# Optimization experiments

Hardware: AMD Instinct MI355X
Metric: run time of the kernel (lower is better)

Reference implementation:

```python
import jax, jax.numpy as jnp
import numpy as np

# PEPS grid configuration (matches init_kwargs)
X, Y = 4, 4            # xnodes, ynodes
D = 6                  # bond_dim
P = 2                  # features_in (physical dim)
F = 10                 # features_out (forced by result.view([10]))
CX, CY = X // 2, Y // 2  # center node carries the output leg
BATCH = 2048


def node_labels(i, j):
    # bond labels after the physical index is contracted away; axis order: up, left, down, right, out
    labs = []
    if i > 0: labs.append(f'v{i-1}_{j}')   # up bond (shared with row i-1)
    if j > 0: labs.append(f'h{i}_{j-1}')   # left bond (shared with col j-1)
    if i < X - 1: labs.append(f'v{i}_{j}') # down bond
    if j < Y - 1: labs.append(f'h{i}_{j}') # right bond
    if (i, j) == (CX, CY): labs.append('o')  # output leg on center node
    return labs


def node_shape(i, j):
    shp = [P]  # physical axis first (input_nodes[i][j][0] ^ peps_nodes[i][j][0])
    shp += [D] * (int(i > 0) + int(j > 0) + int(i < X - 1) + int(j < Y - 1))
    if (i, j) == (CX, CY): shp.append(F)
    return tuple(shp)


def setup_inputs() -> dict:
    key = jax.random.key(0)
    keys = jax.random.split(key, X * Y + 1)
    inp = {"x": jax.random.normal(keys[0], (BATCH, X, Y, P), dtype=jnp.float32)}
    k = 1
    for i in range(X):
        for j in range(Y):
            # simple_peps uniform init with std=0.01
            inp[f"w{i}{j}"] = jax.random.uniform(keys[k], node_shape(i, j), dtype=jnp.float32, minval=-0.01, maxval=0.01)
            k += 1
    return inp


def _td(a, alabs, b, blabs):
    """Label-tracked tensordot over all shared bond labels."""
    shared = [l for l in alabs if l in blabs]
    ai = [alabs.index(l) for l in shared]
    bi = [blabs.index(l) for l in shared]
    out = jnp.tensordot(a, b, axes=(ai, bi))
    labs = [l for l in alabs if l not in shared] + [l for l in blabs if l not in shared]
    return out, labs


def _contract_sample(xs, ws):
    # xs: [X, Y, P] one sample; ws: list-of-lists of node tensors
    # 1) contract each input vector into its PEPS node over the physical axis,
    #    then L2-normalize each contracted node (as in func())
    nodes = []
    for i in range(X):
        row = []
        for j in range(Y):
            t = jnp.tensordot(xs[i, j], ws[i][j], axes=(0, 0))
            t = t / jnp.linalg.norm(t)
            row.append(t)
        nodes.append(row)
    # 2) exact contraction of the 2D network, row-by-row boundary sweep
    cur, labs = nodes[0][0], node_labels(0, 0)
    for j in range(1, Y):
        cur, labs = _td(cur, labs, nodes[0][j], node_labels(0, j))
    for i in range(1, X):
        for j in range(Y):
            cur, labs = _td(cur, labs, nodes[i][j], node_labels(i, j))
    out = cur.reshape(F)  # result.view([10])
    return out / jnp.linalg.norm(out)


def reference(x, w00, w01, w02, w03, w10, w11, w12, w13,
              w20, w21, w22, w23, w30, w31, w32, w33):
    ws = [[w00, w01, w02, w03],
          [w10, w11, w12, w13],
          [w20, w21, w22, w23],
          [w30, w31, w32, w33]]
    return jax.vmap(lambda s: _contract_sample(s, ws))(x)  # [B, F]
```

## Files before the change

### kernel.cpp

```cpp
#include <hip/hip_runtime.h>
#include <math.h>

#define NT 128
#define NTG 256

struct PW { const float* w[16]; int perp[16]; };

__global__ __launch_bounds__(NTG) void gram16(PW pw, float* __restrict__ g) {
    const int n = blockIdx.x;
    const float* __restrict__ W = pw.w[n];
    const int m = pw.perp[n];
    float s00 = 0.f, s01 = 0.f, s11 = 0.f;
    for (int e = threadIdx.x; e < m; e += NTG) {
        float a = W[e], b = W[m + e];
        s00 += a * a; s01 += a * b; s11 += b * b;
    }
    for (int off = 32; off > 0; off >>= 1) {
        s00 += __shfl_down(s00, off, 64);
        s01 += __shfl_down(s01, off, 64);
        s11 += __shfl_down(s11, off, 64);
    }
    __shared__ float red[4][3];
    const int lane = threadIdx.x & 63, wv = threadIdx.x >> 6;
    if (lane == 0) { red[wv][0] = s00; red[wv][1] = s01; red[wv][2] = s11; }
    __syncthreads();
    if (threadIdx.x == 0) {
        float t0 = 0.f, t1 = 0.f, t2 = 0.f;
        for (int i = 0; i < 4; i++) { t0 += red[i][0]; t1 += red[i][1]; t2 += red[i][2]; }
        g[n * 3 + 0] = t0; g[n * 3 + 1] = t1; g[n * 3 + 2] = t2;
    }
}

constexpr int BA = 0, BB = 1296, BC = 2592, BD = 3888;
constexpr int PBo = 5184, SA = 5400, SB = 5616, SC = 5832;
constexpr int ASZ = 5868;

template<int M, int DST>
__device__ __forceinline__ void tmat(float* __restrict__ lds, const float* __restrict__ W,
                                     float al, float be, int tid) {
    for (int e = tid; e < M; e += NT) lds[DST + e] = al * W[e] + be * W[M + e];
}

template<int X1, int X2, int Y1, int Y2, int U, int L, int TX,
         int AX1, int AX2, int AU, int AL,
         int BU, int BLS, int BY1, int BY2,
         int OX1, int OX2, int OY1, int OY2,
         int AOFF, int BOFF, int OOFF>
__device__ __forceinline__ void step(float* __restrict__ lds, int tid) {
    constexpr int XB = X2 / TX;
    constexpr int TILES = X1 * XB * Y1;
    for (int r = tid; r < TILES; r += NT) {
        const int x1 = r / (XB * Y1);
        const int rm = r - x1 * (XB * Y1);
        const int xb = rm / Y1;
        const int y1 = rm - xb * Y1;
        const float* __restrict__ Ab = lds + AOFF + x1 * AX1 + xb * TX * AX2;
        const float* __restrict__ Bb = lds + BOFF + y1 * BY1;
        float acc[TX][Y2];
#pragma unroll
        for (int i = 0; i < TX; i++)
#pragma unroll
            for (int t2 = 0; t2 < Y2; t2++) acc[i][t2] = 0.f;
#pragma unroll
        for (int u = 0; u < U; u++) {
#pragma unroll
            for (int l = 0; l < L; l++) {
                float a[TX];
#pragma unroll
                for (int i = 0; i < TX; i++) a[i] = Ab[i * AX2 + u * AU + l * AL];
                const float* __restrict__ Bp = Bb + u * BU + l * BLS;
#pragma unroll
                for (int t2 = 0; t2 < Y2; t2++) {
                    const float bv = Bp[t2 * BY2];
#pragma unroll
                    for (int i = 0; i < TX; i++) acc[i][t2] += a[i] * bv;
                }
            }
        }
        float* __restrict__ Ob = lds + OOFF + x1 * OX1 + xb * TX * OX2 + y1 * OY1;
#pragma unroll
        for (int i = 0; i < TX; i++)
#pragma unroll
            for (int t2 = 0; t2 < Y2; t2++) Ob[i * OX2 + t2 * OY2] = acc[i][t2];
    }
}

__global__ __launch_bounds__(NT) void peps_main(const float* __restrict__ x, PW pw,
                                                const float* __restrict__ gram,
                                                float* __restrict__ out) {
    __shared__ float lds[ASZ];
    __shared__ float cfa[16], cfb[16];
    __shared__ float red[2][10];

    const int tid = threadIdx.x;
    const int s = blockIdx.x;

    if (tid < 16) {
        const float a = x[s * 32 + tid * 2 + 0];
        const float b = x[s * 32 + tid * 2 + 1];
        const float g0 = gram[tid * 3 + 0], g1 = gram[tid * 3 + 1], g2 = gram[tid * 3 + 2];
        const float inv = 1.f / sqrtf(a * a * g0 + 2.f * a * b * g1 + b * b * g2);
        cfa[tid] = a * inv; cfb[tid] = b * inv;
    }
    __syncthreads();

#define TM(M, DST, WI) tmat<M, DST>(lds, pw.w[WI], cfa[WI], cfb[WI], tid)
#define SYNC __syncthreads()

    TM(36, SC, 0); TM(216, SA, 1); SYNC;
    step<1, 6, 6, 6, 6, 1, 1,  0, 6, 1, 0,   36, 0, 6, 1,   0, 36, 6, 1,  SC, SA, PBo>(lds, tid);
    TM(216, SB, 4); SYNC;
    step<1, 36, 6, 6, 6, 1, 2,  0, 1, 36, 0,  36, 0, 6, 1,   0, 36, 6, 1,  PBo, SB, BA>(lds, tid);
    TM(1296, BB, 5); SYNC;
    step<6, 6, 6, 6, 6, 6, 2,  36, 6, 216, 1, 216, 36, 6, 1, 216, 36, 6, 1, BA, BB, BC>(lds, tid);
    TM(216, SA, 2); TM(36, SC, 3); SYNC;
    step<1, 36, 1, 6, 6, 1, 1,  0, 6, 1, 0,   6, 0, 0, 1,    0, 6, 0, 1,   SA, SC, PBo>(lds, tid);
    TM(216, SB, 7); SYNC;
    step<1, 36, 6, 6, 6, 1, 2,  0, 6, 1, 0,   36, 0, 6, 1,   0, 36, 6, 1,  PBo, SB, BA>(lds, tid);
    TM(1296, BB, 6); SYNC;
    step<6, 6, 6, 6, 6, 6, 2,  36, 6, 216, 1, 36, 6, 216, 1, 216, 36, 6, 1, BB, BA, BD>(lds, tid);
    TM(36, SC, 12); TM(216, SA, 8); SYNC;
    step<6, 6, 6, 6, 6, 6, 2,  36, 6, 216, 1, 6, 216, 36, 1, 216, 36, 6, 1, BC, BD, BA>(lds, tid);
    step<1, 6, 6, 6, 6, 1, 1,  0, 1, 6, 0,    6, 0, 36, 1,   0, 36, 6, 1,  SC, SA, PBo>(lds, tid);
    TM(216, SB, 13); SYNC;
    step<1, 36, 6, 6, 6, 1, 2,  0, 1, 36, 0,  6, 0, 36, 1,   0, 36, 6, 1,  PBo, SB, BC>(lds, tid);
    TM(1296, BD, 9); SYNC;
    step<6, 6, 6, 6, 6, 6, 2,  216, 1, 36, 6, 36, 6, 216, 1, 216, 36, 6, 1, BC, BD, BB>(lds, tid);
    TM(216, SA, 11); TM(36, SC, 15); SYNC;
    step<6, 6, 6, 6, 6, 6, 2,  6, 1, 216, 36, 216, 6, 36, 1, 216, 36, 6, 1, BA, BB, BC>(lds, tid);
    step<6, 6, 1, 6, 6, 1, 1,  36, 6, 1, 0,   6, 0, 0, 1,    36, 6, 0, 1,  SA, SC, PBo>(lds, tid);
    TM(216, SB, 14); SYNC;
    step<6, 6, 6, 6, 6, 1, 2,  36, 6, 1, 0,   1, 0, 36, 6,   216, 1, 6, 36, PBo, SB, BA>(lds, tid);
    SYNC;
    step<6, 6, 6, 6, 6, 6, 2,  216, 1, 36, 6, 216, 36, 6, 1, 216, 36, 6, 1, BC, BA, BB>(lds, tid);
    SYNC;
#undef TM
#undef SYNC

    {
        const float al = cfa[10], be = cfb[10];
        const float* __restrict__ w0 = pw.w[10];
        const float* __restrict__ w1 = w0 + 12960;
        float p[10];
#pragma unroll
        for (int o = 0; o < 10; o++) p[o] = 0.f;
        for (int e = tid; e < 1296; e += NT) {
            const float Ev = lds[BB + e];
            const float* __restrict__ q0 = w0 + e * 10;
            const float* __restrict__ q1 = w1 + e * 10;
#pragma unroll
            for (int o = 0; o < 10; o++) p[o] += Ev * (al * q0[o] + be * q1[o]);
        }
#pragma unroll
        for (int o = 0; o < 10; o++)
            for (int off = 32; off > 0; off >>= 1)
                p[o] += __shfl_down(p[o], off, 64);
        const int lane = tid & 63, wv = tid >> 6;
        if (lane == 0) {
#pragma unroll
            for (int o = 0; o < 10; o++) red[wv][o] = p[o];
        }
        __syncthreads();
        if (tid == 0) {
            float r[10];
            float ss = 0.f;
#pragma unroll
            for (int o = 0; o < 10; o++) {
                r[o] = red[0][o] + red[1][o];
                ss += r[o] * r[o];
            }
            const float inv = 1.f / sqrtf(ss);
#pragma unroll
            for (int o = 0; o < 10; o++) out[s * 10 + o] = r[o] * inv;
        }
    }
}

extern "C" void kernel_launch(void* const* d_in, const int* in_sizes, int n_in,
                              void* d_out, int out_size, void* d_ws, size_t ws_size,
                              hipStream_t stream) {
    PW pw;
    for (int k = 0; k < 16; k++) {
        pw.w[k] = (const float*)d_in[1 + k];
        pw.perp[k] = in_sizes[1 + k] / 2;
    }
    float* gram = (float*)d_ws;
    gram16<<<16, NTG, 0, stream>>>(pw, gram);

    const float* x = (const float*)d_in[0];
    const int B = out_size / 10;
    peps_main<<<B, NT, 0, stream>>>(x, pw, gram, (float*)d_out);
}
```

Measured before the change: 159.4 us.

## Precompute per-quadrant corner tables over physical-index combinations, then combine per sample

Adds a tables kernel that contracts each 4-node corner quadrant for all 16 (or 8) combinations of physical-index choices, using only the weights. Each sample then rebuilds its corner boundary tensors as a linear combination of these tables, weighted by products of its normalized input coefficients, and finishes with three 36x36x36 matmuls, handling two samples per block. This replaces most of the per-sample chained contractions with table reads and dense matmuls. The cost is a larger workspace read from global memory per sample and an extra launch.

```diff
diff --git a/kernel.cpp b/kernel.cpp
--- a/kernel.cpp
+++ b/kernel.cpp
@@ -5,6 +5,11 @@
 #define NTG 256
 
 struct PW { const float* w[16]; int perp[16]; };
+
+#define TLT 64
+#define TRT 20800
+#define BLT 41536
+#define RTT 62272
 
 __global__ __launch_bounds__(NTG) void gram16(PW pw, float* __restrict__ g) {
     const int n = blockIdx.x;
@@ -31,121 +36,219 @@
     }
 }
 
-constexpr int BA = 0, BB = 1296, BC = 2592, BD = 3888;
-constexpr int PBo = 5184, SA = 5400, SB = 5616, SC = 5832;
-constexpr int ASZ = 5868;
+template<int X1, int X2, int Y1, int Y2, int U, int L,
+         int AX1, int AX2, int AU, int AL,
+         int BU, int BLs, int BY1, int BY2,
+         int OX1, int OX2, int OY1, int OY2>
+__device__ __forceinline__ void contract(const float* __restrict__ A,
+                                         const float* __restrict__ Bm,
+                                         float* __restrict__ O, int tid) {
+    constexpr int ROWS = X1 * X2 * Y1;
+    for (int r = tid; r < ROWS; r += NT) {
+        const int x1 = r / (X2 * Y1);
+        const int rm = r - x1 * (X2 * Y1);
+        const int x2 = rm / Y1;
+        const int y1 = rm - x2 * Y1;
+        const float* __restrict__ Ab = A + x1 * AX1 + x2 * AX2;
+        const float* __restrict__ Bb = Bm + y1 * BY1;
+        float acc[Y2];
+#pragma unroll
+        for (int t = 0; t < Y2; t++) acc[t] = 0.f;
+#pragma unroll
+        for (int u = 0; u < U; u++) {
+#pragma unroll
+            for (int l = 0; l < L; l++) {
+                const float a = Ab[u * AU + l * AL];
+                const float* __restrict__ Bp = Bb + u * BU + l * BLs;
+#pragma unroll
+                for (int t = 0; t < Y2; t++) acc[t] += a * Bp[t * BY2];
+            }
+        }
+        float* __restrict__ Ob = O + x1 * OX1 + x2 * OX2 + y1 * OY1;
+#pragma unroll
+        for (int t = 0; t < Y2; t++) Ob[t * OY2] = acc[t];
+    }
+}
 
 template<int M, int DST>
-__device__ __forceinline__ void tmat(float* __restrict__ lds, const float* __restrict__ W,
-                                     float al, float be, int tid) {
-    for (int e = tid; e < M; e += NT) lds[DST + e] = al * W[e] + be * W[M + e];
-}
-
-template<int X1, int X2, int Y1, int Y2, int U, int L, int TX,
-         int AX1, int AX2, int AU, int AL,
-         int BU, int BLS, int BY1, int BY2,
-         int OX1, int OX2, int OY1, int OY2,
-         int AOFF, int BOFF, int OOFF>
-__device__ __forceinline__ void step(float* __restrict__ lds, int tid) {
-    constexpr int XB = X2 / TX;
-    constexpr int TILES = X1 * XB * Y1;
-    for (int r = tid; r < TILES; r += NT) {
-        const int x1 = r / (XB * Y1);
-        const int rm = r - x1 * (XB * Y1);
-        const int xb = rm / Y1;
-        const int y1 = rm - xb * Y1;
-        const float* __restrict__ Ab = lds + AOFF + x1 * AX1 + xb * TX * AX2;
-        const float* __restrict__ Bb = lds + BOFF + y1 * BY1;
-        float acc[TX][Y2];
-#pragma unroll
-        for (int i = 0; i < TX; i++)
-#pragma unroll
-            for (int t2 = 0; t2 < Y2; t2++) acc[i][t2] = 0.f;
-#pragma unroll
-        for (int u = 0; u < U; u++) {
-#pragma unroll
-            for (int l = 0; l < L; l++) {
-                float a[TX];
-#pragma unroll
-                for (int i = 0; i < TX; i++) a[i] = Ab[i * AX2 + u * AU + l * AL];
-                const float* __restrict__ Bp = Bb + u * BU + l * BLS;
-#pragma unroll
-                for (int t2 = 0; t2 < Y2; t2++) {
-                    const float bv = Bp[t2 * BY2];
-#pragma unroll
-                    for (int i = 0; i < TX; i++) acc[i][t2] += a[i] * bv;
-                }
+__device__ __forceinline__ void csel(float* __restrict__ L, const float* __restrict__ W, int tid) {
+    for (int e = tid; e < M; e += NT) L[DST + e] = W[e];
+}
+
+__global__ __launch_bounds__(NT) void tables_k(PW pw, float* __restrict__ ws) {
+    __shared__ float L[4356];
+    constexpr int bA = 0, bB = 1296, bC = 2592, sA = 3888, sB = 4104, sC = 4320;
+    const int tid = threadIdx.x, bid = blockIdx.x;
+    if (bid < 16) {
+        const int p = bid;
+        csel<36, sC>(L, pw.w[0] + ((p >> 0) & 1) * 36, tid);
+        csel<216, sA>(L, pw.w[1] + ((p >> 1) & 1) * 216, tid);
+        __syncthreads();
+        contract<1,6,6,6,6,1,  0,6,1,0,  36,0,6,1,  0,36,6,1>(L+sC, L+sA, L+sB, tid);
+        csel<216, bA>(L, pw.w[4] + ((p >> 2) & 1) * 216, tid);
+        __syncthreads();
+        contract<1,36,6,6,6,1,  0,1,36,0,  36,0,6,1,  0,36,6,1>(L+sB, L+bA, L+bB, tid);
+        csel<1296, bC>(L, pw.w[5] + ((p >> 3) & 1) * 1296, tid);
+        __syncthreads();
+        contract<6,6,6,6,6,6,  36,6,216,1,  216,36,6,1,  216*16,6*16,1*16,36*16>(L+bB, L+bC, ws + TLT + p, tid);
+    } else if (bid < 32) {
+        const int p = bid - 16;
+        csel<216, sA>(L, pw.w[2] + ((p >> 0) & 1) * 216, tid);
+        csel<36, sC>(L, pw.w[3] + ((p >> 1) & 1) * 36, tid);
+        __syncthreads();
+        contract<1,36,1,6,6,1,  0,6,1,0,  6,0,0,1,  0,6,0,1>(L+sA, L+sC, L+sB, tid);
+        csel<216, bA>(L, pw.w[7] + ((p >> 2) & 1) * 216, tid);
+        __syncthreads();
+        contract<1,36,6,6,6,1,  0,6,1,0,  36,0,6,1,  0,36,6,1>(L+sB, L+bA, L+bB, tid);
+        csel<1296, bC>(L, pw.w[6] + ((p >> 3) & 1) * 1296, tid);
+        __syncthreads();
+        contract<6,6,6,6,6,6,  36,6,216,1,  36,6,216,1,  36*16,6*16,216*16,1*16>(L+bC, L+bB, ws + TRT + p, tid);
+    } else if (bid < 48) {
+        const int p = bid - 32;
+        csel<36, sC>(L, pw.w[12] + ((p >> 0) & 1) * 36, tid);
+        csel<216, sA>(L, pw.w[8] + ((p >> 1) & 1) * 216, tid);
+        __syncthreads();
+        contract<1,6,6,6,6,1,  0,1,6,0,  6,0,36,1,  0,36,6,1>(L+sC, L+sA, L+sB, tid);
+        csel<216, bA>(L, pw.w[13] + ((p >> 2) & 1) * 216, tid);
+        __syncthreads();
+        contract<1,36,6,6,6,1,  0,1,36,0,  6,0,36,1,  0,36,6,1>(L+sB, L+bA, L+bB, tid);
+        csel<1296, bC>(L, pw.w[9] + ((p >> 3) & 1) * 1296, tid);
+        __syncthreads();
+        contract<6,6,6,6,6,6,  216,1,36,6,  36,6,216,1,  216*16,1*16,36*16,6*16>(L+bB, L+bC, ws + BLT + p, tid);
+    } else {
+        const int p = bid - 48;
+        csel<216, sA>(L, pw.w[11] + ((p >> 0) & 1) * 216, tid);
+        csel<36, sC>(L, pw.w[15] + ((p >> 1) & 1) * 36, tid);
+        __syncthreads();
+        contract<6,6,1,6,6,1,  36,6,1,0,  6,0,0,1,  36,6,0,1>(L+sA, L+sC, L+sB, tid);
+        csel<216, bA>(L, pw.w[14] + ((p >> 2) & 1) * 216, tid);
+        __syncthreads();
+        contract<6,6,6,6,6,1,  36,6,1,0,  1,0,36,6,  216*8,1*8,6*8,36*8>(L+sB, L+bA, ws + RTT + p, tid);
+    }
+}
+
+constexpr int AR = 5184;
+
+template<int PC, int DST, int GOFF>
+__device__ __forceinline__ void sweep(float* __restrict__ lds, const float* __restrict__ tab,
+                                      const float* __restrict__ gam, int tid) {
+    float g0[PC], g1[PC];
+#pragma unroll
+    for (int c = 0; c < PC; c++) { g0[c] = gam[GOFF + c]; g1[c] = gam[56 + GOFF + c]; }
+    for (int e = tid; e < 1296; e += NT) {
+        const float4* __restrict__ tp = (const float4*)(tab + e * PC);
+        float a0 = 0.f, a1 = 0.f;
+#pragma unroll
+        for (int c = 0; c < PC / 4; c++) {
+            const float4 v = tp[c];
+            a0 += v.x * g0[4*c] + v.y * g0[4*c+1] + v.z * g0[4*c+2] + v.w * g0[4*c+3];
+            a1 += v.x * g1[4*c] + v.y * g1[4*c+1] + v.z * g1[4*c+2] + v.w * g1[4*c+3];
+        }
+        lds[DST + e] = a0;
+        lds[AR + DST + e] = a1;
+    }
+}
+
+template<int SXH, int SXL, int SYH, int SYL, int AOFF, int BOFF, int OOFF>
+__device__ __forceinline__ void kmm(float* __restrict__ lds, int tid) {
+    for (int t = tid; t < 108; t += NT) {
+        const int sl = t / 54;
+        const int r = t - sl * 54;
+        const int xg = r / 3, yg = r - xg * 3;
+        const int x0 = xg * 2, y0 = yg * 12;
+        const float* __restrict__ A = lds + sl * AR + AOFF;
+        const float* __restrict__ B = lds + sl * AR + BOFF;
+        float acc0[12], acc1[12];
+#pragma unroll
+        for (int j = 0; j < 12; j++) { acc0[j] = 0.f; acc1[j] = 0.f; }
+#pragma unroll
+        for (int k = 0; k < 36; k++) {
+            const float2 a = *(const float2*)(A + k * 36 + x0);
+            const float* __restrict__ Bp = B + k * 36 + y0;
+            const float4 v0 = *(const float4*)(Bp);
+            const float4 v1 = *(const float4*)(Bp + 4);
+            const float4 v2 = *(const float4*)(Bp + 8);
+            const float bv[12] = {v0.x,v0.y,v0.z,v0.w, v1.x,v1.y,v1.z,v1.w, v2.x,v2.y,v2.z,v2.w};
+#pragma unroll
+            for (int j = 0; j < 12; j++) {
+                acc0[j] += a.x * bv[j];
+                acc1[j] += a.y * bv[j];
             }
         }
-        float* __restrict__ Ob = lds + OOFF + x1 * OX1 + xb * TX * OX2 + y1 * OY1;
-#pragma unroll
-        for (int i = 0; i < TX; i++)
-#pragma unroll
-            for (int t2 = 0; t2 < Y2; t2++) Ob[i * OX2 + t2 * OY2] = acc[i][t2];
+        float* __restrict__ O = lds + sl * AR + OOFF;
+#pragma unroll
+        for (int i = 0; i < 2; i++) {
+            const int xx = x0 + i;
+            const int xh = xx / 6, xl = xx - xh * 6;
+#pragma unroll
+            for (int j = 0; j < 12; j++) {
+                const int yy = y0 + j;
+                const int yh = yy / 6, yl = yy - yh * 6;
+                O[xh * SXH + xl * SXL + yh * SYH + yl * SYL] = (i == 0) ? acc0[j] : acc1[j];
+            }
+        }
     }
 }
 
 __global__ __launch_bounds__(NT) void peps_main(const float* __restrict__ x, PW pw,
-                                                const float* __restrict__ gram,
+                                                const float* __restrict__ ws,
                                                 float* __restrict__ out) {
-    __shared__ float lds[ASZ];
-    __shared__ float cfa[16], cfb[16];
-    __shared__ float red[2][10];
+    __shared__ float arena[2 * AR];
+    __shared__ float cfa[2][16], cfb[2][16];
+    __shared__ float gam[2 * 56];
 
     const int tid = threadIdx.x;
-    const int s = blockIdx.x;
-
-    if (tid < 16) {
-        const float a = x[s * 32 + tid * 2 + 0];
-        const float b = x[s * 32 + tid * 2 + 1];
-        const float g0 = gram[tid * 3 + 0], g1 = gram[tid * 3 + 1], g2 = gram[tid * 3 + 2];
-        const float inv = 1.f / sqrtf(a * a * g0 + 2.f * a * b * g1 + b * b * g2);
-        cfa[tid] = a * inv; cfb[tid] = b * inv;
-    }
-    __syncthreads();
-
-#define TM(M, DST, WI) tmat<M, DST>(lds, pw.w[WI], cfa[WI], cfb[WI], tid)
-#define SYNC __syncthreads()
-
-    TM(36, SC, 0); TM(216, SA, 1); SYNC;
-    step<1, 6, 6, 6, 6, 1, 1,  0, 6, 1, 0,   36, 0, 6, 1,   0, 36, 6, 1,  SC, SA, PBo>(lds, tid);
-    TM(216, SB, 4); SYNC;
-    step<1, 36, 6, 6, 6, 1, 2,  0, 1, 36, 0,  36, 0, 6, 1,   0, 36, 6, 1,  PBo, SB, BA>(lds, tid);
-    TM(1296, BB, 5); SYNC;
-    step<6, 6, 6, 6, 6, 6, 2,  36, 6, 216, 1, 216, 36, 6, 1, 216, 36, 6, 1, BA, BB, BC>(lds, tid);
-    TM(216, SA, 2); TM(36, SC, 3); SYNC;
-    step<1, 36, 1, 6, 6, 1, 1,  0, 6, 1, 0,   6, 0, 0, 1,    0, 6, 0, 1,   SA, SC, PBo>(lds, tid);
-    TM(216, SB, 7); SYNC;
-    step<1, 36, 6, 6, 6, 1, 2,  0, 6, 1, 0,   36, 0, 6, 1,   0, 36, 6, 1,  PBo, SB, BA>(lds, tid);
-    TM(1296, BB, 6); SYNC;
-    step<6, 6, 6, 6, 6, 6, 2,  36, 6, 216, 1, 36, 6, 216, 1, 216, 36, 6, 1, BB, BA, BD>(lds, tid);
-    TM(36, SC, 12); TM(216, SA, 8); SYNC;
-    step<6, 6, 6, 6, 6, 6, 2,  36, 6, 216, 1, 6, 216, 36, 1, 216, 36, 6, 1, BC, BD, BA>(lds, tid);
-    step<1, 6, 6, 6, 6, 1, 1,  0, 1, 6, 0,    6, 0, 36, 1,   0, 36, 6, 1,  SC, SA, PBo>(lds, tid);
-    TM(216, SB, 13); SYNC;
-    step<1, 36, 6, 6, 6, 1, 2,  0, 1, 36, 0,  6, 0, 36, 1,   0, 36, 6, 1,  PBo, SB, BC>(lds, tid);
-    TM(1296, BD, 9); SYNC;
-    step<6, 6, 6, 6, 6, 6, 2,  216, 1, 36, 6, 36, 6, 216, 1, 216, 36, 6, 1, BC, BD, BB>(lds, tid);
-    TM(216, SA, 11); TM(36, SC, 15); SYNC;
-    step<6, 6, 6, 6, 6, 6, 2,  6, 1, 216, 36, 216, 6, 36, 1, 216, 36, 6, 1, BA, BB, BC>(lds, tid);
-    step<6, 6, 1, 6, 6, 1, 1,  36, 6, 1, 0,   6, 0, 0, 1,    36, 6, 0, 1,  SA, SC, PBo>(lds, tid);
-    TM(216, SB, 14); SYNC;
-    step<6, 6, 6, 6, 6, 1, 2,  36, 6, 1, 0,   1, 0, 36, 6,   216, 1, 6, 36, PBo, SB, BA>(lds, tid);
-    SYNC;
-    step<6, 6, 6, 6, 6, 6, 2,  216, 1, 36, 6, 216, 36, 6, 1, 216, 36, 6, 1, BC, BA, BB>(lds, tid);
-    SYNC;
-#undef TM
-#undef SYNC
+    const int s0 = blockIdx.x * 2;
+    const float* __restrict__ gram = ws;
+
+    if (tid < 32) {
+        const int sl = tid >> 4, n = tid & 15;
+        const float a = x[(s0 + sl) * 32 + n * 2 + 0];
+        const float b = x[(s0 + sl) * 32 + n * 2 + 1];
+        const float g0 = gram[n*3+0], g1 = gram[n*3+1], g2 = gram[n*3+2];
+        const float inv = 1.f / sqrtf(a*a*g0 + 2.f*a*b*g1 + b*b*g2);
+        cfa[sl][n] = a * inv; cfb[sl][n] = b * inv;
+    }
+    __syncthreads();
+
+    if (tid < 112) {
+        const int sl = tid / 56, u = tid - sl * 56;
+        int p, nl0, nl1, nl2, nl3, nb;
+        if (u < 16)      { p = u;      nl0 = 0;  nl1 = 1;  nl2 = 4;  nl3 = 5; nb = 4; }
+        else if (u < 32) { p = u - 16; nl0 = 2;  nl1 = 3;  nl2 = 7;  nl3 = 6; nb = 4; }
+        else if (u < 48) { p = u - 32; nl0 = 12; nl1 = 8;  nl2 = 13; nl3 = 9; nb = 4; }
+        else             { p = u - 48; nl0 = 11; nl1 = 15; nl2 = 14; nl3 = 0; nb = 3; }
+        float gv = ((p >> 0) & 1) ? cfb[sl][nl0] : cfa[sl][nl0];
+        gv      *= ((p >> 1) & 1) ? cfb[sl][nl1] : cfa[sl][nl1];
+        gv      *= ((p >> 2) & 1) ? cfb[sl][nl2] : cfa[sl][nl2];
+        if (nb == 4) gv *= ((p >> 3) & 1) ? cfb[sl][nl3] : cfa[sl][nl3];
+        gam[sl * 56 + u] = gv;
+    }
+    __syncthreads();
+
+    sweep<16, 0,    0>(arena, ws + TLT, gam, tid);
+    sweep<16, 1296, 16>(arena, ws + TRT, gam, tid);
+    sweep<16, 3888, 32>(arena, ws + BLT, gam, tid);
+    __syncthreads();
+    kmm<216, 36, 6, 1,  0, 1296, 2592>(arena, tid);
+    __syncthreads();
+    kmm<6, 216, 1, 36,  2592, 3888, 0>(arena, tid);
+    sweep<8, 1296, 48>(arena, ws + RTT, gam, tid);
+    __syncthreads();
+    kmm<216, 36, 6, 1,  0, 1296, 2592>(arena, tid);
+    __syncthreads();
 
     {
-        const float al = cfa[10], be = cfb[10];
+        const int lane = tid & 63, sl = tid >> 6;
+        const float al = cfa[sl][10], be = cfb[sl][10];
         const float* __restrict__ w0 = pw.w[10];
         const float* __restrict__ w1 = w0 + 12960;
+        const float* __restrict__ E = arena + sl * AR + 2592;
         float p[10];
 #pragma unroll
         for (int o = 0; o < 10; o++) p[o] = 0.f;
-        for (int e = tid; e < 1296; e += NT) {
-            const float Ev = lds[BB + e];
+        for (int e = lane; e < 1296; e += 64) {
+            const float Ev = E[e];
             const float* __restrict__ q0 = w0 + e * 10;
             const float* __restrict__ q1 = w1 + e * 10;
 #pragma unroll
@@ -155,23 +258,13 @@
         for (int o = 0; o < 10; o++)
             for (int off = 32; off > 0; off >>= 1)
                 p[o] += __shfl_down(p[o], off, 64);
-        const int lane = tid & 63, wv = tid >> 6;
         if (lane == 0) {
-#pragma unroll
-            for (int o = 0; o < 10; o++) red[wv][o] = p[o];
-        }
-        __syncthreads();
-        if (tid == 0) {
-            float r[10];
             float ss = 0.f;
 #pragma unroll
-            for (int o = 0; o < 10; o++) {
-                r[o] = red[0][o] + red[1][o];
-                ss += r[o] * r[o];
-            }
+            for (int o = 0; o < 10; o++) ss += p[o] * p[o];
             const float inv = 1.f / sqrtf(ss);
 #pragma unroll
-            for (int o = 0; o < 10; o++) out[s * 10 + o] = r[o] * inv;
+            for (int o = 0; o < 10; o++) out[(s0 + sl) * 10 + o] = p[o] * inv;
         }
     }
 }
@@ -184,10 +277,11 @@
         pw.w[k] = (const float*)d_in[1 + k];
         pw.perp[k] = in_sizes[1 + k] / 2;
     }
-    float* gram = (float*)d_ws;
-    gram16<<<16, NTG, 0, stream>>>(pw, gram);
+    float* ws = (float*)d_ws;
+    gram16<<<16, NTG, 0, stream>>>(pw, ws);
+    tables_k<<<56, NT, 0, stream>>>(pw, ws);
 
     const float* x = (const float*)d_in[0];
     const int B = out_size / 10;
-    peps_main<<<B, NT, 0, stream>>>(x, pw, gram, (float*)d_out);
-}
+    peps_main<<<B / 2, NT, 0, stream>>>(x, pw, ws, (float*)d_out);
+}
```

Result: slower. 169.0 us (+6.1%).
